# Optimization experiments

Measured on AMD Instinct MI355X. Metric: run time of the kernel, lower is better.

The kernel has to match this reference:

```python
import jax, jax.numpy as jnp
import numpy as np

B, T, C, H = 128, 512, 256, 64  # batch, seq (<= BLOCK_SIZE=512), EMBED_SIZE, HEAD_SIZE


def setup_inputs() -> dict:
    key = jax.random.key(0)
    k0, k1, k2, k3 = jax.random.split(key, 4)
    # nn.Linear(C, H, bias=False) applies x @ W.T with W:[H,C]; we store the
    # transposed weight [C,H] so the math x @ W is identical.
    scale = 1.0 / np.sqrt(C)  # rough Linear-init scale, values only matter for testing
    return {
        "input_embeddings": jax.random.normal(k0, (B, T, C), dtype=jnp.float32),
        "Wq": jax.random.normal(k1, (C, H), dtype=jnp.float32) * scale,
        "Wk": jax.random.normal(k2, (C, H), dtype=jnp.float32) * scale,
        "Wv": jax.random.normal(k3, (C, H), dtype=jnp.float32) * scale,
    }


def reference(input_embeddings, Wq, Wk, Wv):
    x = input_embeddings
    t = x.shape[1]
    h = Wq.shape[1]
    q = jnp.einsum("btc,ch->bth", x, Wq)
    k = jnp.einsum("btc,ch->bth", x, Wk)
    v = jnp.einsum("btc,ch->bth", x, Wv)
    # QK^T / sqrt(H), causal mask, softmax  (faithful to masked_fill(-inf))
    sim = jnp.einsum("bth,bsh->bts", q, k) / jnp.sqrt(jnp.asarray(h, x.dtype))
    causal = jnp.tril(jnp.ones((t, t), dtype=bool))
    sim = jnp.where(causal, sim, -jnp.inf)
    wei = jax.nn.softmax(sim, axis=-1)
    out = jnp.einsum("bts,bsh->bth", wei, v)
    return out
```

## Files before the change

kernel.cpp:

```cpp
#include <hip/hip_runtime.h>
#include <hip/hip_bf16.h>
#include <math.h>

#define Bn 128
#define Tn 512
#define Cn 256
#define Hn 64
#define NQKV 192
#define XP 264
#define HP2 72
#define SCL 0.18033688011112042f

typedef __attribute__((ext_vector_type(8))) short short8v;
typedef __attribute__((ext_vector_type(4))) float float4v;

__device__ __forceinline__ ushort f2bf(float f) {
    __hip_bfloat16 h = __float2bfloat16(f);
    return *reinterpret_cast<ushort*>(&h);
}

__global__ __launch_bounds__(256) void prep_w_kernel(
    const float* __restrict__ Wq, const float* __restrict__ Wk,
    const float* __restrict__ Wv, ushort* __restrict__ wcT)
{
    const int col = blockIdx.x;
    const int c   = threadIdx.x;
    const float* W = (col < 64) ? Wq : (col < 128) ? Wk : Wv;
    const int h = col & 63;
    wcT[col * Cn + (c ^ ((col & 7) << 3))] = f2bf(W[c * Hn + h]);
}

__global__ __launch_bounds__(512) void qkv_mfma_kernel(
    const float* __restrict__ x, const ushort* __restrict__ wcT,
    ushort* __restrict__ q, ushort* __restrict__ k, ushort* __restrict__ vT)
{
    __shared__ char lds[148480];
    const int XOFF = 98304;
    const int BOFF = 132096;

    const int tid  = threadIdx.x;
    const int lane = tid & 63;
    const int wv   = tid >> 6;
    const int lr   = lane & 15;
    const int hi   = lane >> 4;
    const int s    = wv & 3;
    const int hh   = wv >> 2;
    const long row0 = (long)blockIdx.x * 64;

    {
        const char* gw = (const char*)wcT;
        #pragma unroll
        for (int i = 0; i < 12; ++i) {
            int off = (wv * 12 + i) * 1024;
            __builtin_amdgcn_global_load_lds(
                (const __attribute__((address_space(1))) unsigned int*)(gw + off + (lane << 4)),
                (__attribute__((address_space(3))) unsigned int*)(lds + off),
                16, 0, 0);
        }
    }

    {
        const float4* x4 = (const float4*)(x + row0 * Cn);
        float4 xr[8];
        #pragma unroll
        for (int i = 0; i < 8; ++i) xr[i] = x4[tid + i * 512];
        #pragma unroll
        for (int i = 0; i < 8; ++i) {
            int idx = tid + i * 512;
            int r   = idx >> 6;
            int c4  = idx & 63;
            union { ushort u[4]; uint2 p; } pk;
            pk.u[0] = f2bf(xr[i].x); pk.u[1] = f2bf(xr[i].y);
            pk.u[2] = f2bf(xr[i].z); pk.u[3] = f2bf(xr[i].w);
            *(uint2*)(lds + XOFF + r * 528 + c4 * 8) = pk.p;
        }
    }
    __syncthreads();

    float4v aqk[4], av[2];
    #pragma unroll
    for (int j = 0; j < 4; ++j) aqk[j] = (float4v){0.f, 0.f, 0.f, 0.f};
    av[0] = (float4v){0.f, 0.f, 0.f, 0.f};
    av[1] = av[0];

    const char* xrow = lds + XOFF + (s * 16 + lr) * 528 + hi * 16;
    const int wxor = (lr & 7) << 4;
    #pragma unroll
    for (int ks = 0; ks < 8; ++ks) {
        const int kb = (ks * 64 + hi * 16);
        short8v xa = *(const short8v*)(xrow + ks * 64);
        #pragma unroll
        for (int j = 0; j < 4; ++j) {
            short8v wf = *(const short8v*)(lds + (hh * 64 + j * 16 + lr) * 512 + (kb ^ wxor));
            aqk[j] = __builtin_amdgcn_mfma_f32_16x16x32_bf16(wf, xa, aqk[j], 0, 0, 0);
        }
        #pragma unroll
        for (int j = 0; j < 2; ++j) {
            short8v wf = *(const short8v*)(lds + (128 + hh * 32 + j * 16 + lr) * 512 + (kb ^ wxor));
            av[j] = __builtin_amdgcn_mfma_f32_16x16x32_bf16(xa, wf, av[j], 0, 0, 0);
        }
    }

    {
        const int bb = (int)(row0 >> 9);
        const int tl = (int)(row0 & 511) + s * 16 + hi * 4;
        #pragma unroll
        for (int j = 0; j < 2; ++j) {
            int h = hh * 32 + j * 16 + lr;
            ushort4 pk;
            pk.x = f2bf(av[j][0]); pk.y = f2bf(av[j][1]);
            pk.z = f2bf(av[j][2]); pk.w = f2bf(av[j][3]);
            *(ushort4*)(vT + ((long)bb * Hn + h) * Tn + tl) = pk;
        }
    }

    {
        char* bnc = lds + BOFF + wv * 2048;
        #pragma unroll
        for (int j = 0; j < 4; ++j) {
            ushort4 pk;
            pk.x = f2bf(aqk[j][0]); pk.y = f2bf(aqk[j][1]);
            pk.z = f2bf(aqk[j][2]); pk.w = f2bf(aqk[j][3]);
            *(ushort4*)(bnc + lr * 128 + ((j * 32 + hi * 8) ^ ((lr & 7) << 4))) = pk;
        }
        ushort* dst = hh ? k : q;
        #pragma unroll
        for (int i = 0; i < 2; ++i) {
            int t = i * 8 + (lane >> 3);
            int c = lane & 7;
            uint4 w = *(const uint4*)(bnc + t * 128 + ((c * 16) ^ ((t & 7) << 4)));
            *(uint4*)(dst + (row0 + s * 16 + t) * Hn + c * 8) = w;
        }
    }
}

__global__ __launch_bounds__(512) void attn_mfma_kernel(
    const ushort* __restrict__ q, const ushort* __restrict__ k,
    const ushort* __restrict__ vT, float* __restrict__ out)
{
    __shared__ ushort Ks[64 * HP2];
    __shared__ ushort Vt[64 * HP2];
    __shared__ ushort Pl[8][16 * HP2];

    const int tid = threadIdx.x;
    const int f   = blockIdx.x;
    const int c   = f & 255;
    const int b   = c >> 1;
    const int par = c & 1;
    const int qtp = (f < 256) ? par : (3 - par);
    const int ntiles = 2 * qtp + 2;

    const long base  = (long)b * Tn * Hn;
    const int lane = tid & 63;
    const int wv   = tid >> 6;
    const int lr   = lane & 15;
    const int hi   = lane >> 4;

    const int qrow_g = qtp * 128 + wv * 16;
    const int mrow0  = qrow_g + hi * 4;

    short8v qa[2];
    {
        const ushort* qp = q + base + (long)(qrow_g + lr) * Hn + hi * 8;
        qa[0] = *(const short8v*)(qp);
        qa[1] = *(const short8v*)(qp + 32);
    }

    const int sr  = tid >> 3;
    const int sc8 = tid & 7;
    uint4 kreg = *(const uint4*)(k + base + (long)sr * Hn + sc8 * 8);
    uint4 vreg = *(const uint4*)(vT + base + (long)sr * Tn + sc8 * 8);

    float4v o[4];
    #pragma unroll
    for (int n = 0; n < 4; ++n) o[n] = (float4v){0.f, 0.f, 0.f, 0.f};
    float m[4], l[4];
    #pragma unroll
    for (int reg = 0; reg < 4; ++reg) { m[reg] = -INFINITY; l[reg] = 0.f; }

    for (int kt = 0; kt < ntiles; ++kt) {
        __syncthreads();
        *(uint4*)&Ks[sr * HP2 + sc8 * 8] = kreg;
        *(uint4*)&Vt[sr * HP2 + sc8 * 8] = vreg;
        __syncthreads();
        if (kt + 1 < ntiles) {
            kreg = *(const uint4*)(k  + base + (long)((kt + 1) * 64 + sr) * Hn + sc8 * 8);
            vreg = *(const uint4*)(vT + base + (long)sr * Tn + (kt + 1) * 64 + sc8 * 8);
        }
        if (kt * 64 > qrow_g + 15) continue;

        float4v s4[4];
        #pragma unroll
        for (int n = 0; n < 4; ++n) s4[n] = (float4v){0.f, 0.f, 0.f, 0.f};
        #pragma unroll
        for (int ks = 0; ks < 2; ++ks) {
            short8v a = qa[ks];
            #pragma unroll
            for (int n = 0; n < 4; ++n) {
                short8v bb = *(const short8v*)&Ks[(n * 16 + lr) * HP2 + ks * 32 + hi * 8];
                s4[n] = __builtin_amdgcn_mfma_f32_16x16x32_bf16(a, bb, s4[n], 0, 0, 0);
            }
        }

        const bool partial = (kt * 64 + 63 > qrow_g);
        if (partial) {
            #pragma unroll
            for (int n = 0; n < 4; ++n) {
                int kcol = kt * 64 + n * 16 + lr;
                #pragma unroll
                for (int reg = 0; reg < 4; ++reg) {
                    float y = s4[n][reg] * SCL;
                    s4[n][reg] = (kcol <= mrow0 + reg) ? y : -INFINITY;
                }
            }
        } else {
            #pragma unroll
            for (int n = 0; n < 4; ++n)
                #pragma unroll
                for (int reg = 0; reg < 4; ++reg) s4[n][reg] *= SCL;
        }

        #pragma unroll
        for (int reg = 0; reg < 4; ++reg) {
            float mx = fmaxf(fmaxf(s4[0][reg], s4[1][reg]),
                             fmaxf(s4[2][reg], s4[3][reg]));
            mx = fmaxf(mx, __shfl_xor(mx, 1));
            mx = fmaxf(mx, __shfl_xor(mx, 2));
            mx = fmaxf(mx, __shfl_xor(mx, 4));
            mx = fmaxf(mx, __shfl_xor(mx, 8));
            float mN = fmaxf(m[reg], mx);
            float sc = exp2f(m[reg] - mN);
            float ps = 0.f;
            #pragma unroll
            for (int n = 0; n < 4; ++n) {
                float p = exp2f(s4[n][reg] - mN);
                s4[n][reg] = p;
                ps += p;
            }
            ps += __shfl_xor(ps, 1);
            ps += __shfl_xor(ps, 2);
            ps += __shfl_xor(ps, 4);
            ps += __shfl_xor(ps, 8);
            l[reg] = l[reg] * sc + ps;
            m[reg] = mN;
            #pragma unroll
            for (int n = 0; n < 4; ++n) o[n][reg] *= sc;
        }

        #pragma unroll
        for (int n = 0; n < 4; ++n)
            #pragma unroll
            for (int reg = 0; reg < 4; ++reg)
                Pl[wv][(hi * 4 + reg) * HP2 + n * 16 + lr] = f2bf(s4[n][reg]);

        #pragma unroll
        for (int ks = 0; ks < 2; ++ks) {
            short8v a = *(const short8v*)&Pl[wv][lr * HP2 + ks * 32 + hi * 8];
            #pragma unroll
            for (int n = 0; n < 4; ++n) {
                short8v bb = *(const short8v*)&Vt[(n * 16 + lr) * HP2 + ks * 32 + hi * 8];
                o[n] = __builtin_amdgcn_mfma_f32_16x16x32_bf16(a, bb, o[n], 0, 0, 0);
            }
        }
    }

    #pragma unroll
    for (int reg = 0; reg < 4; ++reg) {
        float inv = 1.0f / l[reg];
        float* orow = out + base + (long)(mrow0 + reg) * Hn;
        #pragma unroll
        for (int n = 0; n < 4; ++n)
            orow[n * 16 + lr] = o[n][reg] * inv;
    }
}

extern "C" void kernel_launch(void* const* d_in, const int* in_sizes, int n_in,
                              void* d_out, int out_size, void* d_ws, size_t ws_size,
                              hipStream_t stream) {
    const float* x  = (const float*)d_in[0];
    const float* Wq = (const float*)d_in[1];
    const float* Wk = (const float*)d_in[2];
    const float* Wv = (const float*)d_in[3];
    float* out = (float*)d_out;

    const size_t n = (size_t)Bn * Tn * Hn;
    ushort* qws = (ushort*)d_ws;
    ushort* kws = qws + n;
    ushort* vTs = kws + n;
    ushort* wcT = vTs + n;

    prep_w_kernel<<<dim3(NQKV), 256, 0, stream>>>(Wq, Wk, Wv, wcT);
    qkv_mfma_kernel<<<dim3(Bn * Tn / 64), 512, 0, stream>>>(x, wcT, qws, kws, vTs);
    attn_mfma_kernel<<<dim3(512), 512, 0, stream>>>(qws, kws, vTs, out);
}
```

Baseline: 57.04 us.

## Split QKV projection across two half-width blocks to cut LDS and raise occupancy

Each QKV projection block now computes only half of the output columns (Q plus half of V, or K plus the other half of V) with 256 threads, and the grid doubles to 2048 blocks. The weight buffer is reordered so each half is contiguous, and the x tile in LDS uses an XOR swizzle instead of padding. The bounce buffer reuses the x region after an added barrier. LDS per block drops from about 148KB to 80KB, which should allow more blocks per CU, but every x tile is now loaded and converted twice.

Result: faster. 51.46 us (-9.8%).

```diff
diff --git a/kernel.cpp b/kernel.cpp
--- a/kernel.cpp
+++ b/kernel.cpp
@@ -6,8 +6,6 @@
 #define Tn 512
 #define Cn 256
 #define Hn 64
-#define NQKV 192
-#define XP 264
 #define HP2 72
 #define SCL 0.18033688011112042f
 
@@ -21,34 +19,39 @@
 
 __global__ __launch_bounds__(256) void prep_w_kernel(
     const float* __restrict__ Wq, const float* __restrict__ Wk,
-    const float* __restrict__ Wv, ushort* __restrict__ wcT)
+    const float* __restrict__ Wv, ushort* __restrict__ wcT2)
 {
-    const int col = blockIdx.x;
+    const int row = blockIdx.x;
     const int c   = threadIdx.x;
-    const float* W = (col < 64) ? Wq : (col < 128) ? Wk : Wv;
-    const int h = col & 63;
-    wcT[col * Cn + (c ^ ((col & 7) << 3))] = f2bf(W[c * Hn + h]);
-}
-
-__global__ __launch_bounds__(512) void qkv_mfma_kernel(
-    const float* __restrict__ x, const ushort* __restrict__ wcT,
+    const int nh  = row / 96;
+    const int rr  = row % 96;
+    const int scol = (nh == 0) ? (rr < 64 ? rr : 128 + (rr - 64))
+                               : (rr < 64 ? 64 + rr : 160 + (rr - 64));
+    const float* W = (scol < 64) ? Wq : (scol < 128) ? Wk : Wv;
+    const int h = scol & 63;
+    wcT2[row * Cn + (c ^ ((rr & 7) << 3))] = f2bf(W[c * Hn + h]);
+}
+
+__global__ __launch_bounds__(256) void qkv_mfma_kernel(
+    const float* __restrict__ x, const ushort* __restrict__ wcT2,
     ushort* __restrict__ q, ushort* __restrict__ k, ushort* __restrict__ vT)
 {
-    __shared__ char lds[148480];
-    const int XOFF = 98304;
-    const int BOFF = 132096;
+    __shared__ char lds[81920];
+    const int XOFF = 49152;
 
     const int tid  = threadIdx.x;
     const int lane = tid & 63;
     const int wv   = tid >> 6;
     const int lr   = lane & 15;
     const int hi   = lane >> 4;
-    const int s    = wv & 3;
-    const int hh   = wv >> 2;
-    const long row0 = (long)blockIdx.x * 64;
-
-    {
-        const char* gw = (const char*)wcT;
+
+    const int bid     = blockIdx.x;
+    const int nh      = (bid >> 3) & 1;
+    const int rowtile = (bid & 7) | ((bid >> 4) << 3);
+    const long rows0  = (long)rowtile * 64;
+
+    {
+        const char* gw = (const char*)wcT2 + (long)nh * 96 * 512;
         #pragma unroll
         for (int i = 0; i < 12; ++i) {
             int off = (wv * 12 + i) * 1024;
@@ -60,19 +63,20 @@
     }
 
     {
-        const float4* x4 = (const float4*)(x + row0 * Cn);
-        float4 xr[8];
-        #pragma unroll
-        for (int i = 0; i < 8; ++i) xr[i] = x4[tid + i * 512];
-        #pragma unroll
-        for (int i = 0; i < 8; ++i) {
-            int idx = tid + i * 512;
+        const float4* x4 = (const float4*)(x + rows0 * Cn);
+        float4 xr[16];
+        #pragma unroll
+        for (int i = 0; i < 16; ++i) xr[i] = x4[tid + i * 256];
+        #pragma unroll
+        for (int i = 0; i < 16; ++i) {
+            int idx = tid + i * 256;
             int r   = idx >> 6;
             int c4  = idx & 63;
             union { ushort u[4]; uint2 p; } pk;
             pk.u[0] = f2bf(xr[i].x); pk.u[1] = f2bf(xr[i].y);
             pk.u[2] = f2bf(xr[i].z); pk.u[3] = f2bf(xr[i].w);
-            *(uint2*)(lds + XOFF + r * 528 + c4 * 8) = pk.p;
+            int off = (r * 512 + c4 * 8) ^ ((r & 7) << 4);
+            *(uint2*)(lds + XOFF + off) = pk.p;
         }
     }
     __syncthreads();
@@ -83,30 +87,30 @@
     av[0] = (float4v){0.f, 0.f, 0.f, 0.f};
     av[1] = av[0];
 
-    const char* xrow = lds + XOFF + (s * 16 + lr) * 528 + hi * 16;
-    const int wxor = (lr & 7) << 4;
+    const int xrow = wv * 16 + lr;
+    const int xxor = (lr & 7) << 4;
     #pragma unroll
     for (int ks = 0; ks < 8; ++ks) {
-        const int kb = (ks * 64 + hi * 16);
-        short8v xa = *(const short8v*)(xrow + ks * 64);
+        const int kb = ks * 64 + hi * 16;
+        short8v xa = *(const short8v*)(lds + XOFF + ((xrow * 512 + kb) ^ xxor));
         #pragma unroll
         for (int j = 0; j < 4; ++j) {
-            short8v wf = *(const short8v*)(lds + (hh * 64 + j * 16 + lr) * 512 + (kb ^ wxor));
+            short8v wf = *(const short8v*)(lds + (j * 16 + lr) * 512 + (kb ^ xxor));
             aqk[j] = __builtin_amdgcn_mfma_f32_16x16x32_bf16(wf, xa, aqk[j], 0, 0, 0);
         }
         #pragma unroll
         for (int j = 0; j < 2; ++j) {
-            short8v wf = *(const short8v*)(lds + (128 + hh * 32 + j * 16 + lr) * 512 + (kb ^ wxor));
+            short8v wf = *(const short8v*)(lds + (64 + j * 16 + lr) * 512 + (kb ^ xxor));
             av[j] = __builtin_amdgcn_mfma_f32_16x16x32_bf16(xa, wf, av[j], 0, 0, 0);
         }
     }
 
     {
-        const int bb = (int)(row0 >> 9);
-        const int tl = (int)(row0 & 511) + s * 16 + hi * 4;
+        const int bb = (int)(rows0 >> 9);
+        const int tl = (int)(rows0 & 511) + wv * 16 + hi * 4;
         #pragma unroll
         for (int j = 0; j < 2; ++j) {
-            int h = hh * 32 + j * 16 + lr;
+            int h = nh * 32 + j * 16 + lr;
             ushort4 pk;
             pk.x = f2bf(av[j][0]); pk.y = f2bf(av[j][1]);
             pk.z = f2bf(av[j][2]); pk.w = f2bf(av[j][3]);
@@ -114,8 +118,10 @@
         }
     }
 
-    {
-        char* bnc = lds + BOFF + wv * 2048;
+    __syncthreads();
+
+    {
+        char* bnc = lds + XOFF + wv * 2048;
         #pragma unroll
         for (int j = 0; j < 4; ++j) {
             ushort4 pk;
@@ -123,13 +129,13 @@
             pk.z = f2bf(aqk[j][2]); pk.w = f2bf(aqk[j][3]);
             *(ushort4*)(bnc + lr * 128 + ((j * 32 + hi * 8) ^ ((lr & 7) << 4))) = pk;
         }
-        ushort* dst = hh ? k : q;
+        ushort* dst = nh ? k : q;
         #pragma unroll
         for (int i = 0; i < 2; ++i) {
             int t = i * 8 + (lane >> 3);
             int c = lane & 7;
             uint4 w = *(const uint4*)(bnc + t * 128 + ((c * 16) ^ ((t & 7) << 4)));
-            *(uint4*)(dst + (row0 + s * 16 + t) * Hn + c * 8) = w;
+            *(uint4*)(dst + (rows0 + wv * 16 + t) * Hn + c * 8) = w;
         }
     }
 }
@@ -284,12 +290,12 @@
     float* out = (float*)d_out;
 
     const size_t n = (size_t)Bn * Tn * Hn;
-    ushort* qws = (ushort*)d_ws;
-    ushort* kws = qws + n;
-    ushort* vTs = kws + n;
-    ushort* wcT = vTs + n;
-
-    prep_w_kernel<<<dim3(NQKV), 256, 0, stream>>>(Wq, Wk, Wv, wcT);
-    qkv_mfma_kernel<<<dim3(Bn * Tn / 64), 512, 0, stream>>>(x, wcT, qws, kws, vTs);
+    ushort* qws  = (ushort*)d_ws;
+    ushort* kws  = qws + n;
+    ushort* vTs  = kws + n;
+    ushort* wcT2 = vTs + n;
+
+    prep_w_kernel<<<dim3(192), 256, 0, stream>>>(Wq, Wk, Wv, wcT2);
+    qkv_mfma_kernel<<<dim3(2048), 256, 0, stream>>>(x, wcT2, qws, kws, vTs);
     attn_mfma_kernel<<<dim3(512), 512, 0, stream>>>(qws, kws, vTs, out);
 }
```
